# Kernel tuning notes

Hardware: AMD Instinct MI355X
Metric: run time of the kernel (lower is better)

## Reference

```python
import jax, jax.numpy as jnp
import numpy as np

BS, NA, NE_, NL = 128, 3, 3, 3
NALL = NA - 1                 # n_allies
ENT = NA + NE_ + NL           # 9 entities
EM1 = ENT - 1                 # 8
HID = 64                      # hidden_dim
HEAD = 4
HIN = 9                       # hyper input dim
HYP = 64                      # hyper hidden dim
NRBF, RUB = 3, 10.0
EPS = 1e-7


def _lin_init(k, fan_in, fan_out):
    k1, k2 = jax.random.split(k)
    lim = 1.0 / np.sqrt(fan_in)
    w = jax.random.uniform(k1, (fan_in, fan_out), minval=-lim, maxval=lim, dtype=jnp.float32)
    b = jax.random.uniform(k2, (fan_out,), minval=-lim, maxval=lim, dtype=jnp.float32)
    return w, b


def setup_inputs():
    key = jax.random.key(0)
    ks = jax.random.split(key, 12)
    d = {}
    obs_dim = 4 + 2 * (NL + NALL + NE_) + 2 * (NALL + NE_)  # 30
    d["inputs"] = jax.random.normal(ks[0], (BS * NA, obs_dim), dtype=jnp.float32)
    d["hidden_state"] = jnp.zeros((1, HID), dtype=jnp.float32)
    d["actions"] = jax.random.normal(ks[1], (BS * NA, 2), dtype=jnp.float32)
    out_dim = (HIN + 1) * HID * HEAD  # 2560
    d["hA1_w"], d["hA1_b"] = _lin_init(ks[2], HIN, HYP)
    d["hA2_w"], d["hA2_b"] = _lin_init(ks[3], HYP, out_dim)
    d["hE1_w"], d["hE1_b"] = _lin_init(ks[4], HIN, HYP)
    d["hE2_w"], d["hE2_b"] = _lin_init(ks[5], HYP, out_dim)
    d["hL1_w"], d["hL1_b"] = _lin_init(ks[6], HIN, HYP)
    d["hL2_w"], d["hL2_b"] = _lin_init(ks[7], HYP, out_dim)
    d["merger_w"] = jnp.ones((1, HEAD, HID), dtype=jnp.float32)
    d["fc1_w"], d["fc1_b"] = _lin_init(ks[8], HID + 3, HID)
    d["fc2_w"], d["fc2_b"] = _lin_init(ks[9], HID, 1)
    return d


def _pair_out(feat, w1, b1, w2, b2):
    # hypernetwork: Linear(9,64) -> LeakyReLU -> Linear(64, (9+1)*64*4)
    h = jax.nn.leaky_relu(feat @ w1 + b1, negative_slope=0.01)
    out = h @ w2 + b2                               # (bs,NA,EM1,EM1,2560)
    nw = HIN * HID * HEAD
    w = out[..., :nw].reshape(feat.shape[:-1] + (HIN, HID * HEAD))
    b = out[..., nw:]
    y = jnp.einsum('...k,...kd->...d', feat, w) + b  # tiny 1x9 @ 9x256 per pair
    return y.reshape(feat.shape[:-1] + (HEAD, HID))


def _forward(inputs, actions, hA1_w, hA1_b, hA2_w, hA2_b, hE1_w, hE1_b, hE2_w, hE2_b,
             hL1_w, hL1_b, hL2_w, hL2_b, merger_w, fc1_w, fc1_b, fc2_w, fc2_b):
    bs = inputs.shape[0] // NA
    ob = inputs
    own = ob[:, :4].reshape(bs, NA, 4)
    i = 4
    lm_pos = ob[:, i:i + NL * 2].reshape(bs, NA, NL, 2); i += NL * 2
    ally_pos = ob[:, i:i + NALL * 2].reshape(bs, NA, NALL, 2); i += NALL * 2
    enemy_pos = ob[:, i:i + NE_ * 2].reshape(bs, NA, NE_, 2); i += NE_ * 2
    entity_pos = jnp.concatenate([ally_pos, enemy_pos, lm_pos], axis=-2)  # (bs,NA,EM1,2)
    ally_vel = ob[:, i:i + NALL * 2].reshape(bs, NA, NALL, 2); i += NALL * 2
    enemy_vel = ob[:, i:i + NE_ * 2].reshape(bs, NA, NE_, 2)
    lm_vel = jnp.zeros_like(lm_pos) - own[:, :, None, :2]
    entity_vel = jnp.concatenate([ally_vel, enemy_vel, lm_vel], axis=-2)  # (bs,NA,EM1,2)
    # rel_vel[b,a,j,i] = vel[i] - vel[j]
    rel_vel = entity_vel[:, :, None, :, :] - entity_vel[:, :, :, None, :]
    vel_norm = jnp.sqrt((entity_vel ** 2).sum(-1))
    sin_a = entity_vel[..., 1] / (vel_norm + EPS)
    cos_a = entity_vel[..., 0] / (vel_norm + EPS)
    act = actions.reshape(bs, NA, 2)
    act_norm = jnp.sqrt((act ** 2).sum(-1))        # (bs,NA)
    sin_b = act[..., 1] / (act_norm + EPS)
    cos_b = act[..., 0] / (act_norm + EPS)
    dist = jnp.sqrt((entity_pos ** 2).sum(-1))     # (bs,NA,EM1)
    sin_t = entity_pos[..., 1] / (dist + EPS)
    cos_t = entity_pos[..., 0] / (dist + EPS)
    # pair angles: A,C vary over last axis (i), B over second-to-last (j)
    sA, cA = sin_t[:, :, None, :], cos_t[:, :, None, :]
    sB, cB = sin_t[:, :, :, None], cos_t[:, :, :, None]
    sC, cC = sin_a[:, :, None, :], cos_a[:, :, None, :]
    angle_info = jnp.stack([sA * cB - cA * sB, cA * cB + sA * sB,
                            sC * cB - cC * sB, cC * cB + sC * sB], axis=-1)
    angle_info = jnp.broadcast_to(angle_info, (bs, NA, EM1, EM1, 4))
    sD, cD = sin_b[:, :, None], cos_b[:, :, None]
    act_angle = jnp.stack([sD * cos_t - cD * sin_t, cD * cos_t + sD * sin_t], axis=-1)  # (bs,NA,EM1,2)
    # gaussian RBF (schnet-style smearing, num_rbf=3, rbound_upper=10)
    offset = jnp.linspace(0.0, RUB, NRBF)
    coeff = -0.5 / (offset[1] - offset[0]) ** 2
    rbf = jnp.exp(coeff * (dist[..., None] - offset) ** 2)  # (bs,NA,EM1,NRBF)
    feat_dist = jnp.broadcast_to(rbf[:, :, None, :, :], (bs, NA, EM1, EM1, NRBF))
    feat = jnp.concatenate([feat_dist, angle_info, rel_vel], axis=-1)  # (bs,NA,EM1,EM1,9)
    ally_out = _pair_out(feat, hA1_w, hA1_b, hA2_w, hA2_b)
    enemy_out = _pair_out(feat, hE1_w, hE1_b, hE2_w, hE2_b)
    lm_out = _pair_out(feat, hL1_w, hL1_b, hL2_w, hL2_b)
    # type-based selection over the source-entity axis (dim 3), then sum-aggregate
    m = jnp.concatenate([ally_out[:, :, :, :NALL],
                         enemy_out[:, :, :, NALL:NALL + NE_],
                         lm_out[:, :, :, NALL + NE_:]], axis=3)
    m_sum = m.sum(axis=3)                               # (bs,NA,EM1,HEAD,HID)
    mw = jax.nn.softmax(merger_w, axis=1)               # (1,HEAD,HID)
    m_jki = (mw * m_sum).sum(axis=-2)                   # (bs,NA,EM1,HID)
    an = jnp.broadcast_to(act_norm[:, :, None], (bs, NA, EM1))[..., None]
    final = jnp.concatenate([m_jki, an, act_angle], axis=-1)  # (bs,NA,EM1,HID+3)
    x = jax.nn.relu(final)
    x = jax.nn.relu(x @ fc1_w + fc1_b)
    q = (x @ fc2_w + fc2_b).mean(axis=-2).reshape(-1, 1)  # (bs*NA,1)
    return q, x


def reference(inputs, hidden_state, actions, hA1_w, hA1_b, hA2_w, hA2_b,
              hE1_w, hE1_b, hE2_w, hE2_b, hL1_w, hL1_b, hL2_w, hL2_b,
              merger_w, fc1_w, fc1_b, fc2_w, fc2_b):
    q, x = _forward(inputs, actions, hA1_w, hA1_b, hA2_w, hA2_b,
                    hE1_w, hE1_b, hE2_w, hE2_b, hL1_w, hL1_b, hL2_w, hL2_b,
                    merger_w, fc1_w, fc1_b, fc2_w, fc2_b)
    return q, x
```

## Files before the change

### kernel.cpp

```cpp
#include <hip/hip_runtime.h>
#include <math.h>

#define EPS 1e-7f
#define NETS 3
#define HROWP 384
#define HG    (HROWP/4)
#define GPW   (HG/4)
#define JSTRIDE (NETS*HROWP)
#define W2R_F4_TOT (2*NETS*HG*64)
#define ZPART_OFF 589824

__global__ __launch_bounds__(256) void prep_w2r(
    const float* __restrict__ W2A, const float* __restrict__ b2A,
    const float* __restrict__ W2E, const float* __restrict__ b2E,
    const float* __restrict__ W2L, const float* __restrict__ b2L,
    const float* __restrict__ merger, float* __restrict__ W2r)
{
    int idx = blockIdx.x * 256 + threadIdx.x;
    if (idx >= W2R_F4_TOT) return;
    int half = idx / (NETS*HG*64);
    int rem  = idx - half * (NETS*HG*64);
    int net  = rem / (HG*64);
    rem     -= net * (HG*64);
    int g4   = rem >> 6;
    int hid  = rem & 63;

    float m0 = merger[hid], m1 = merger[64+hid], m2 = merger[128+hid], m3 = merger[192+hid];
    float mx = fmaxf(fmaxf(m0, m1), fmaxf(m2, m3));
    float e0 = expf(m0-mx), e1 = expf(m1-mx), e2 = expf(m2-mx), e3 = expf(m3-mx);
    float inv = 1.0f / (e0+e1+e2+e3);
    float w0 = e0*inv, w1 = e1*inv, w2 = e2*inv, w3 = e3*inv;

    const float* W2 = (net==0) ? W2A : ((net==1) ? W2E : W2L);
    const float* b2 = (net==0) ? b2A : ((net==1) ? b2E : b2L);

    float4 v;
    float* vp = &v.x;
    #pragma unroll
    for (int r = 0; r < 4; ++r) {
        int row = g4*4 + r;
        float val = 0.0f;
        if (row < 325) {
            const float* src;
            int kk;
            if (row < 320) { kk = half*5 + (row >> 6); int h = row & 63; src = W2 + h*2560; }
            else           { kk = half*5 + (row - 320);                  src = b2; }
            int col = (kk < 9) ? kk*256 : 2304;
            val = w0*src[col+hid] + w1*src[col+64+hid] + w2*src[col+128+hid] + w3*src[col+192+hid];
        }
        vp[r] = val;
    }
    ((float4*)W2r)[idx] = v;
}

__global__ __launch_bounds__(256, 3) void half_kernel(
    const float* __restrict__ inputs, const float* __restrict__ actions,
    const float* __restrict__ W1A, const float* __restrict__ b1A,
    const float* __restrict__ W1E, const float* __restrict__ b1E,
    const float* __restrict__ W1L, const float* __restrict__ b1L,
    const float* __restrict__ W2r, float* __restrict__ Zpart)
{
    __shared__ float sOb[32];
    __shared__ float sSt[8], sCt[8], sSa[8], sCa[8], sVx[8], sVy[8];
    __shared__ float sRbf[8][3];
    __shared__ __align__(16) float sF2[64][12];
    __shared__ __align__(16) float sU[8 * JSTRIDE];

    const int tid   = threadIdx.x;
    const int agent = blockIdx.x >> 1;
    const int half  = blockIdx.x & 1;
    const int lane  = tid & 63;
    const int w     = tid >> 6;

    float w1r[3][9], b1r[3];
    {
        const float* Ws[3] = {W1A, W1E, W1L};
        const float* bs[3] = {b1A, b1E, b1L};
        #pragma unroll
        for (int net = 0; net < 3; ++net) {
            #pragma unroll
            for (int kk = 0; kk < 9; ++kk) w1r[net][kk] = Ws[net][kk*64 + lane];
            b1r[net] = bs[net][lane];
        }
    }

    if (tid < 30) sOb[tid] = inputs[agent*30 + tid];
    if (tid == 30) sOb[30] = actions[agent*2 + 0];
    if (tid == 31) sOb[31] = actions[agent*2 + 1];
    __syncthreads();

    if (tid < 8) {
        int e = tid;
        float px, py, vx, vy;
        if (e < 2)      {           px = sOb[10+2*e]; py = sOb[11+2*e]; vx = sOb[20+2*e]; vy = sOb[21+2*e]; }
        else if (e < 5) { int t=e-2; px = sOb[14+2*t]; py = sOb[15+2*t]; vx = sOb[24+2*t]; vy = sOb[25+2*t]; }
        else            { int t=e-5; px = sOb[4+2*t];  py = sOb[5+2*t];  vx = -sOb[0];     vy = -sOb[1]; }
        float d  = sqrtf(px*px + py*py);
        sSt[e] = py / (d + EPS);
        sCt[e] = px / (d + EPS);
        float vn = sqrtf(vx*vx + vy*vy);
        sSa[e] = vy / (vn + EPS);
        sCa[e] = vx / (vn + EPS);
        sVx[e] = vx; sVy[e] = vy;
        sRbf[e][0] = expf(-0.02f * d * d);
        float d5  = d - 5.0f;  sRbf[e][1] = expf(-0.02f * d5  * d5);
        float d10 = d - 10.0f; sRbf[e][2] = expf(-0.02f * d10 * d10);
    }
    __syncthreads();

    if (tid < 64) {
        int p = tid, j = p >> 3, k = p & 7;
        sF2[p][0] = sRbf[k][0];
        sF2[p][1] = sRbf[k][1];
        sF2[p][2] = sRbf[k][2];
        sF2[p][3] = sSt[k]*sCt[j] - sCt[k]*sSt[j];
        sF2[p][4] = sCt[k]*sCt[j] + sSt[k]*sSt[j];
        sF2[p][5] = sSa[k]*sCt[j] - sCa[k]*sSt[j];
        sF2[p][6] = sCa[k]*sCt[j] + sSa[k]*sSt[j];
        sF2[p][7] = sVx[k] - sVx[j];
        sF2[p][8] = sVy[k] - sVy[j];
        sF2[p][9] = 1.0f;
        sF2[p][10] = 0.0f;
        sF2[p][11] = 0.0f;
    }
    __syncthreads();

    {
        const int h = lane;
        #pragma unroll
        for (int t = 0; t < 2; ++t) {
            int j = 2*w + t;
            #pragma unroll
            for (int net = 0; net < NETS; ++net) {
                int ks = (net==0) ? 0 : ((net==1) ? 2 : 5);
                int kn = (net==0) ? 2 : 3;
                float v0=0.f,v1=0.f,v2=0.f,v3=0.f,v4=0.f;
                float gs0=0.f,gs1=0.f,gs2=0.f,gs3=0.f,gs4=0.f;
                for (int q = 0; q < kn; ++q) {
                    int p = j*8 + ks + q;
                    float4 fa = *(const float4*)&sF2[p][0];
                    float4 fb = *(const float4*)&sF2[p][4];
                    float4 fc = *(const float4*)&sF2[p][8];
                    float acc = b1r[net];
                    acc = fmaf(fa.x, w1r[net][0], acc);
                    acc = fmaf(fa.y, w1r[net][1], acc);
                    acc = fmaf(fa.z, w1r[net][2], acc);
                    acc = fmaf(fa.w, w1r[net][3], acc);
                    acc = fmaf(fb.x, w1r[net][4], acc);
                    acc = fmaf(fb.y, w1r[net][5], acc);
                    acc = fmaf(fb.z, w1r[net][6], acc);
                    acc = fmaf(fb.w, w1r[net][7], acc);
                    acc = fmaf(fc.x, w1r[net][8], acc);
                    float H = (acc > 0.0f) ? acc : 0.01f*acc;
                    float g0 = half ? fb.y : fa.x;
                    float g1 = half ? fb.z : fa.y;
                    float g2 = half ? fb.w : fa.z;
                    float g3 = half ? fc.x : fa.w;
                    float g4 = half ? fc.y : fb.x;
                    v0 = fmaf(H, g0, v0);  gs0 += g0;
                    v1 = fmaf(H, g1, v1);  gs1 += g1;
                    v2 = fmaf(H, g2, v2);  gs2 += g2;
                    v3 = fmaf(H, g3, v3);  gs3 += g3;
                    v4 = fmaf(H, g4, v4);  gs4 += g4;
                }
                float* dst = sU + (j*NETS + net)*HROWP + h;
                dst[0]   = v0;
                dst[64]  = v1;
                dst[128] = v2;
                dst[192] = v3;
                dst[256] = v4;
                float bv = 0.0f;
                bv = (h==0) ? gs0 : bv;
                bv = (h==1) ? gs1 : bv;
                bv = (h==2) ? gs2 : bv;
                bv = (h==3) ? gs3 : bv;
                bv = (h==4) ? gs4 : bv;
                dst[320 - h + h] = bv;
                sU[(j*NETS + net)*HROWP + 320 + h] = bv;
            }
        }
    }
    __syncthreads();

    float vr[8][4];
    {
        const int q = lane >> 4, hh = lane & 15;
        const int base = w * GPW;
        float acc[8][4];
        #pragma unroll
        for (int j = 0; j < 8; ++j)
            #pragma unroll
            for (int k = 0; k < 4; ++k) acc[j][k] = 0.0f;

        const float4* Wbase = (const float4*)W2r + (size_t)half * (NETS*HG*64);
        float4 wk0, wk1, wk2, wk3;
        {   int g = base + q;
            const float4* wb = Wbase + g*64 + hh;
            wk0 = wb[0]; wk1 = wb[16]; wk2 = wb[32]; wk3 = wb[48]; }

        for (int it = 0; it < 18; ++it) {
            int net = it / 6, u = it - net*6;
            int g = base + u*4 + q;
            float4 nk0, nk1, nk2, nk3;
            if (it < 17) {
                int nit = it + 1;
                int nnet = nit / 6, nu_ = nit - nnet*6;
                int ng = base + nu_*4 + q;
                const float4* wb = Wbase + (nnet*HG + ng)*64 + hh;
                nk0 = wb[0]; nk1 = wb[16]; nk2 = wb[32]; nk3 = wb[48];
            }
            const float* Ub = sU + net*HROWP + g*4;
            #pragma unroll
            for (int j = 0; j < 8; ++j) {
                float4 uu = *(const float4*)(Ub + j*JSTRIDE);
                acc[j][0] = fmaf(uu.x,wk0.x, fmaf(uu.y,wk0.y, fmaf(uu.z,wk0.z, fmaf(uu.w,wk0.w, acc[j][0]))));
                acc[j][1] = fmaf(uu.x,wk1.x, fmaf(uu.y,wk1.y, fmaf(uu.z,wk1.z, fmaf(uu.w,wk1.w, acc[j][1]))));
                acc[j][2] = fmaf(uu.x,wk2.x, fmaf(uu.y,wk2.y, fmaf(uu.z,wk2.z, fmaf(uu.w,wk2.w, acc[j][2]))));
                acc[j][3] = fmaf(uu.x,wk3.x, fmaf(uu.y,wk3.y, fmaf(uu.z,wk3.z, fmaf(uu.w,wk3.w, acc[j][3]))));
            }
            wk0 = nk0; wk1 = nk1; wk2 = nk2; wk3 = nk3;
        }
        #pragma unroll
        for (int j = 0; j < 8; ++j)
            #pragma unroll
            for (int k = 0; k < 4; ++k) {
                float v = acc[j][k];
                v += __shfl_xor(v, 16);
                v += __shfl_xor(v, 32);
                vr[j][k] = v;
            }
    }
    __syncthreads();
    {
        float* sZp = sU;
        const int q = lane >> 4, hh = lane & 15;
        if (q == 0) {
            #pragma unroll
            for (int j = 0; j < 8; ++j)
                #pragma unroll
                for (int k = 0; k < 4; ++k)
                    sZp[(w*8 + j)*64 + k*16 + hh] = vr[j][k];
        }
    }
    __syncthreads();
    {
        const float* sZp = sU;
        float* dst = Zpart + (size_t)agent*1024 + half*512;
        for (int o = tid; o < 512; o += 256)
            dst[o] = sZp[o] + sZp[512+o] + sZp[1024+o] + sZp[1536+o];
    }
}

__global__ __launch_bounds__(256) void epilogue_kernel(
    const float* __restrict__ inputs, const float* __restrict__ actions,
    const float* __restrict__ Zpart,
    const float* __restrict__ fc1w, const float* __restrict__ fc1b,
    const float* __restrict__ fc2w, const float* __restrict__ fc2b,
    float* __restrict__ out_q, float* __restrict__ out_x)
{
    __shared__ float sOb[32];
    __shared__ float sSt[8], sCt[8];
    __shared__ float sAct[3];
    __shared__ float sZ[8][64];
    __shared__ float sRed[4];

    const int tid   = threadIdx.x;
    const int agent = blockIdx.x;

    if (tid < 30) sOb[tid] = inputs[agent*30 + tid];
    if (tid == 30) sOb[30] = actions[agent*2 + 0];
    if (tid == 31) sOb[31] = actions[agent*2 + 1];
    __syncthreads();

    if (tid < 8) {
        int e = tid;
        float px, py;
        if (e < 2)      {           px = sOb[10+2*e]; py = sOb[11+2*e]; }
        else if (e < 5) { int t=e-2; px = sOb[14+2*t]; py = sOb[15+2*t]; }
        else            { int t=e-5; px = sOb[4+2*t];  py = sOb[5+2*t]; }
        float d = sqrtf(px*px + py*py);
        sSt[e] = py / (d + EPS);
        sCt[e] = px / (d + EPS);
    }
    if (tid == 8) {
        float ax = sOb[30], ay = sOb[31];
        float an = sqrtf(ax*ax + ay*ay);
        sAct[0] = an;
        sAct[1] = ay / (an + EPS);
        sAct[2] = ax / (an + EPS);
    }
    const float* Zp = Zpart + (size_t)agent*1024;
    for (int o = tid; o < 512; o += 256) {
        float z = Zp[o] + Zp[512 + o];
        ((float*)sZ)[o] = (z > 0.0f) ? z : 0.0f;
    }
    __syncthreads();

    float an  = sAct[0], sb = sAct[1], cb = sAct[2];
    float anr = (an > 0.0f) ? an : 0.0f;
    float myq = 0.0f;
    #pragma unroll
    for (int i = 0; i < 2; ++i) {
        int o = i*256 + tid;
        int j = o >> 6, c = o & 63;
        float acc = fc1b[c];
        #pragma unroll 8
        for (int d = 0; d < 64; ++d)
            acc = fmaf(sZ[j][d], fc1w[d*64 + c], acc);
        float aa0 = sb*sCt[j] - cb*sSt[j];
        float aa1 = cb*sCt[j] + sb*sSt[j];
        aa0 = (aa0 > 0.0f) ? aa0 : 0.0f;
        aa1 = (aa1 > 0.0f) ? aa1 : 0.0f;
        acc = fmaf(anr, fc1w[64*64 + c], acc);
        acc = fmaf(aa0, fc1w[65*64 + c], acc);
        acc = fmaf(aa1, fc1w[66*64 + c], acc);
        float x1 = (acc > 0.0f) ? acc : 0.0f;
        out_x[(agent*8 + j)*64 + c] = x1;
        myq = fmaf(x1, fc2w[c], myq);
    }
    for (int off = 32; off; off >>= 1) myq += __shfl_down(myq, off);
    int lane = tid & 63, w = tid >> 6;
    if (lane == 0) sRed[w] = myq;
    __syncthreads();
    if (tid == 0) out_q[agent] = (sRed[0] + sRed[1] + sRed[2] + sRed[3]) * 0.125f + fc2b[0];
}

extern "C" void kernel_launch(void* const* d_in, const int* in_sizes, int n_in,
                              void* d_out, int out_size, void* d_ws, size_t ws_size,
                              hipStream_t stream) {
    const float* inputs  = (const float*)d_in[0];
    const float* actions = (const float*)d_in[2];
    const float* hA1_w = (const float*)d_in[3];  const float* hA1_b = (const float*)d_in[4];
    const float* hA2_w = (const float*)d_in[5];  const float* hA2_b = (const float*)d_in[6];
    const float* hE1_w = (const float*)d_in[7];  const float* hE1_b = (const float*)d_in[8];
    const float* hE2_w = (const float*)d_in[9];  const float* hE2_b = (const float*)d_in[10];
    const float* hL1_w = (const float*)d_in[11]; const float* hL1_b = (const float*)d_in[12];
    const float* hL2_w = (const float*)d_in[13]; const float* hL2_b = (const float*)d_in[14];
    const float* merger = (const float*)d_in[15];
    const float* fc1w = (const float*)d_in[16];  const float* fc1b = (const float*)d_in[17];
    const float* fc2w = (const float*)d_in[18];  const float* fc2b = (const float*)d_in[19];

    float* W2r   = (float*)d_ws;
    float* Zpart = (float*)((char*)d_ws + ZPART_OFF);
    float* q     = (float*)d_out;
    float* x     = q + 384;

    prep_w2r<<<(W2R_F4_TOT + 255)/256, 256, 0, stream>>>(
        hA2_w, hA2_b, hE2_w, hE2_b, hL2_w, hL2_b, merger, W2r);
    half_kernel<<<768, 256, 0, stream>>>(
        inputs, actions, hA1_w, hA1_b, hE1_w, hE1_b, hL1_w, hL1_b, W2r, Zpart);
    epilogue_kernel<<<384, 256, 0, stream>>>(
        inputs, actions, Zpart, fc1w, fc1b, fc2w, fc2b, q, x);
}
```

Measured before the change: 120.0 us.

## Compute pair features with wave shuffles and write per-wave partials to global

Pair geometry features are now built entirely in registers with cross-lane shuffles inside each wave, instead of staged through several shared-memory arrays. This removes two block barriers and the shared scratch arrays. The W2 weight prefetch is issued at kernel start so it overlaps the feature computation. The final cross-wave shared reduction and its barriers are also dropped: each wave writes its own partial tile to global memory, and the epilogue kernel sums eight partials instead of two. In exchange, the Zpart scratch buffer grows fourfold and the epilogue does more global reads, so the buffer must be large enough.

After: 121.6 us. About the same (+1.3%).

```diff
diff --git a/kernel.cpp b/kernel.cpp
--- a/kernel.cpp
+++ b/kernel.cpp
@@ -60,10 +60,6 @@
     const float* __restrict__ W1L, const float* __restrict__ b1L,
     const float* __restrict__ W2r, float* __restrict__ Zpart)
 {
-    __shared__ float sOb[32];
-    __shared__ float sSt[8], sCt[8], sSa[8], sCa[8], sVx[8], sVy[8];
-    __shared__ float sRbf[8][3];
-    __shared__ __align__(16) float sF2[64][12];
     __shared__ __align__(16) float sU[8 * JSTRIDE];
 
     const int tid   = threadIdx.x;
@@ -71,6 +67,7 @@
     const int half  = blockIdx.x & 1;
     const int lane  = tid & 63;
     const int w     = tid >> 6;
+    const int q     = lane >> 4, hh = lane & 15;
 
     float w1r[3][9], b1r[3];
     {
@@ -84,170 +81,137 @@
         }
     }
 
-    if (tid < 30) sOb[tid] = inputs[agent*30 + tid];
-    if (tid == 30) sOb[30] = actions[agent*2 + 0];
-    if (tid == 31) sOb[31] = actions[agent*2 + 1];
+    const float4* Wbase = (const float4*)W2r + (size_t)half * (NETS*HG*64);
+    const int base = w * GPW;
+    float4 wk0, wk1, wk2, wk3;
+    {
+        int g = base + q;
+        const float4* wb = Wbase + g*64 + hh;
+        wk0 = wb[0]; wk1 = wb[16]; wk2 = wb[32]; wk3 = wb[48];
+    }
+
+    float ob = 0.0f;
+    if (lane < 30)      ob = inputs[agent*30 + lane];
+    else if (lane < 32) ob = actions[agent*2 + (lane - 30)];
+
+    int e = lane & 7;
+    int ppos, vpos; bool lm = false;
+    if (e < 2)      { ppos = 10+2*e;     vpos = 20+2*e; }
+    else if (e < 5) { ppos = 14+2*(e-2); vpos = 24+2*(e-2); }
+    else            { ppos = 4+2*(e-5);  vpos = 0; lm = true; }
+    float px = __shfl(ob, ppos), py = __shfl(ob, ppos+1);
+    float vx = __shfl(ob, vpos), vy = __shfl(ob, vpos+1);
+    if (lm) { vx = -vx; vy = -vy; }
+    float d  = sqrtf(px*px + py*py);
+    float st = py / (d + EPS), ct = px / (d + EPS);
+    float vn = sqrtf(vx*vx + vy*vy);
+    float sa = vy / (vn + EPS), ca = vx / (vn + EPS);
+    float rb0 = expf(-0.02f * d * d);
+    float d5  = d - 5.0f,  rb1 = expf(-0.02f * d5 * d5);
+    float d10 = d - 10.0f, rb2 = expf(-0.02f * d10 * d10);
+
+    int jj = lane >> 3;
+    float st_j = __shfl(st, jj), ct_j = __shfl(ct, jj);
+    float vx_j = __shfl(vx, jj), vy_j = __shfl(vy, jj);
+    float f0 = rb0, f1 = rb1, f2 = rb2;
+    float f3 = st*ct_j - ct*st_j;
+    float f4 = ct*ct_j + st*st_j;
+    float f5 = sa*ct_j - ca*st_j;
+    float f6 = ca*ct_j + sa*st_j;
+    float f7 = vx - vx_j;
+    float f8 = vy - vy_j;
+
+    #pragma unroll
+    for (int t = 0; t < 2; ++t) {
+        int j = 2*w + t;
+        #pragma unroll
+        for (int net = 0; net < NETS; ++net) {
+            int ks = (net==0) ? 0 : ((net==1) ? 2 : 5);
+            int kn = (net==0) ? 2 : 3;
+            float v0=0.f,v1=0.f,v2=0.f,v3=0.f,v4=0.f;
+            float gs0=0.f,gs1=0.f,gs2=0.f,gs3=0.f,gs4=0.f;
+            for (int qq = 0; qq < kn; ++qq) {
+                int p = j*8 + ks + qq;
+                float s0=__shfl(f0,p), s1=__shfl(f1,p), s2=__shfl(f2,p);
+                float s3=__shfl(f3,p), s4=__shfl(f4,p), s5=__shfl(f5,p);
+                float s6=__shfl(f6,p), s7=__shfl(f7,p), s8=__shfl(f8,p);
+                float acc = b1r[net];
+                acc = fmaf(s0, w1r[net][0], acc);
+                acc = fmaf(s1, w1r[net][1], acc);
+                acc = fmaf(s2, w1r[net][2], acc);
+                acc = fmaf(s3, w1r[net][3], acc);
+                acc = fmaf(s4, w1r[net][4], acc);
+                acc = fmaf(s5, w1r[net][5], acc);
+                acc = fmaf(s6, w1r[net][6], acc);
+                acc = fmaf(s7, w1r[net][7], acc);
+                acc = fmaf(s8, w1r[net][8], acc);
+                float H = (acc > 0.0f) ? acc : 0.01f*acc;
+                float g0 = half ? s5 : s0;
+                float g1 = half ? s6 : s1;
+                float g2 = half ? s7 : s2;
+                float g3 = half ? s8 : s3;
+                float g4 = half ? 1.0f : s4;
+                v0 = fmaf(H, g0, v0);  gs0 += g0;
+                v1 = fmaf(H, g1, v1);  gs1 += g1;
+                v2 = fmaf(H, g2, v2);  gs2 += g2;
+                v3 = fmaf(H, g3, v3);  gs3 += g3;
+                v4 = fmaf(H, g4, v4);  gs4 += g4;
+            }
+            float* dst = sU + (j*NETS + net)*HROWP + lane;
+            dst[0]   = v0;
+            dst[64]  = v1;
+            dst[128] = v2;
+            dst[192] = v3;
+            dst[256] = v4;
+            float bv = 0.0f;
+            bv = (lane==0) ? gs0 : bv;
+            bv = (lane==1) ? gs1 : bv;
+            bv = (lane==2) ? gs2 : bv;
+            bv = (lane==3) ? gs3 : bv;
+            bv = (lane==4) ? gs4 : bv;
+            dst[320] = bv;
+        }
+    }
     __syncthreads();
 
-    if (tid < 8) {
-        int e = tid;
-        float px, py, vx, vy;
-        if (e < 2)      {           px = sOb[10+2*e]; py = sOb[11+2*e]; vx = sOb[20+2*e]; vy = sOb[21+2*e]; }
-        else if (e < 5) { int t=e-2; px = sOb[14+2*t]; py = sOb[15+2*t]; vx = sOb[24+2*t]; vy = sOb[25+2*t]; }
-        else            { int t=e-5; px = sOb[4+2*t];  py = sOb[5+2*t];  vx = -sOb[0];     vy = -sOb[1]; }
-        float d  = sqrtf(px*px + py*py);
-        sSt[e] = py / (d + EPS);
-        sCt[e] = px / (d + EPS);
-        float vn = sqrtf(vx*vx + vy*vy);
-        sSa[e] = vy / (vn + EPS);
-        sCa[e] = vx / (vn + EPS);
-        sVx[e] = vx; sVy[e] = vy;
-        sRbf[e][0] = expf(-0.02f * d * d);
-        float d5  = d - 5.0f;  sRbf[e][1] = expf(-0.02f * d5  * d5);
-        float d10 = d - 10.0f; sRbf[e][2] = expf(-0.02f * d10 * d10);
-    }
-    __syncthreads();
-
-    if (tid < 64) {
-        int p = tid, j = p >> 3, k = p & 7;
-        sF2[p][0] = sRbf[k][0];
-        sF2[p][1] = sRbf[k][1];
-        sF2[p][2] = sRbf[k][2];
-        sF2[p][3] = sSt[k]*sCt[j] - sCt[k]*sSt[j];
-        sF2[p][4] = sCt[k]*sCt[j] + sSt[k]*sSt[j];
-        sF2[p][5] = sSa[k]*sCt[j] - sCa[k]*sSt[j];
-        sF2[p][6] = sCa[k]*sCt[j] + sSa[k]*sSt[j];
-        sF2[p][7] = sVx[k] - sVx[j];
-        sF2[p][8] = sVy[k] - sVy[j];
-        sF2[p][9] = 1.0f;
-        sF2[p][10] = 0.0f;
-        sF2[p][11] = 0.0f;
-    }
-    __syncthreads();
-
-    {
-        const int h = lane;
-        #pragma unroll
-        for (int t = 0; t < 2; ++t) {
-            int j = 2*w + t;
-            #pragma unroll
-            for (int net = 0; net < NETS; ++net) {
-                int ks = (net==0) ? 0 : ((net==1) ? 2 : 5);
-                int kn = (net==0) ? 2 : 3;
-                float v0=0.f,v1=0.f,v2=0.f,v3=0.f,v4=0.f;
-                float gs0=0.f,gs1=0.f,gs2=0.f,gs3=0.f,gs4=0.f;
-                for (int q = 0; q < kn; ++q) {
-                    int p = j*8 + ks + q;
-                    float4 fa = *(const float4*)&sF2[p][0];
-                    float4 fb = *(const float4*)&sF2[p][4];
-                    float4 fc = *(const float4*)&sF2[p][8];
-                    float acc = b1r[net];
-                    acc = fmaf(fa.x, w1r[net][0], acc);
-                    acc = fmaf(fa.y, w1r[net][1], acc);
-                    acc = fmaf(fa.z, w1r[net][2], acc);
-                    acc = fmaf(fa.w, w1r[net][3], acc);
-                    acc = fmaf(fb.x, w1r[net][4], acc);
-                    acc = fmaf(fb.y, w1r[net][5], acc);
-                    acc = fmaf(fb.z, w1r[net][6], acc);
-                    acc = fmaf(fb.w, w1r[net][7], acc);
-                    acc = fmaf(fc.x, w1r[net][8], acc);
-                    float H = (acc > 0.0f) ? acc : 0.01f*acc;
-                    float g0 = half ? fb.y : fa.x;
-                    float g1 = half ? fb.z : fa.y;
-                    float g2 = half ? fb.w : fa.z;
-                    float g3 = half ? fc.x : fa.w;
-                    float g4 = half ? fc.y : fb.x;
-                    v0 = fmaf(H, g0, v0);  gs0 += g0;
-                    v1 = fmaf(H, g1, v1);  gs1 += g1;
-                    v2 = fmaf(H, g2, v2);  gs2 += g2;
-                    v3 = fmaf(H, g3, v3);  gs3 += g3;
-                    v4 = fmaf(H, g4, v4);  gs4 += g4;
-                }
-                float* dst = sU + (j*NETS + net)*HROWP + h;
-                dst[0]   = v0;
-                dst[64]  = v1;
-                dst[128] = v2;
-                dst[192] = v3;
-                dst[256] = v4;
-                float bv = 0.0f;
-                bv = (h==0) ? gs0 : bv;
-                bv = (h==1) ? gs1 : bv;
-                bv = (h==2) ? gs2 : bv;
-                bv = (h==3) ? gs3 : bv;
-                bv = (h==4) ? gs4 : bv;
-                dst[320 - h + h] = bv;
-                sU[(j*NETS + net)*HROWP + 320 + h] = bv;
-            }
-        }
-    }
-    __syncthreads();
-
-    float vr[8][4];
-    {
-        const int q = lane >> 4, hh = lane & 15;
-        const int base = w * GPW;
-        float acc[8][4];
-        #pragma unroll
-        for (int j = 0; j < 8; ++j)
-            #pragma unroll
-            for (int k = 0; k < 4; ++k) acc[j][k] = 0.0f;
-
-        const float4* Wbase = (const float4*)W2r + (size_t)half * (NETS*HG*64);
-        float4 wk0, wk1, wk2, wk3;
-        {   int g = base + q;
-            const float4* wb = Wbase + g*64 + hh;
-            wk0 = wb[0]; wk1 = wb[16]; wk2 = wb[32]; wk3 = wb[48]; }
-
-        for (int it = 0; it < 18; ++it) {
-            int net = it / 6, u = it - net*6;
-            int g = base + u*4 + q;
-            float4 nk0, nk1, nk2, nk3;
-            if (it < 17) {
-                int nit = it + 1;
-                int nnet = nit / 6, nu_ = nit - nnet*6;
-                int ng = base + nu_*4 + q;
-                const float4* wb = Wbase + (nnet*HG + ng)*64 + hh;
-                nk0 = wb[0]; nk1 = wb[16]; nk2 = wb[32]; nk3 = wb[48];
-            }
-            const float* Ub = sU + net*HROWP + g*4;
-            #pragma unroll
-            for (int j = 0; j < 8; ++j) {
-                float4 uu = *(const float4*)(Ub + j*JSTRIDE);
-                acc[j][0] = fmaf(uu.x,wk0.x, fmaf(uu.y,wk0.y, fmaf(uu.z,wk0.z, fmaf(uu.w,wk0.w, acc[j][0]))));
-                acc[j][1] = fmaf(uu.x,wk1.x, fmaf(uu.y,wk1.y, fmaf(uu.z,wk1.z, fmaf(uu.w,wk1.w, acc[j][1]))));
-                acc[j][2] = fmaf(uu.x,wk2.x, fmaf(uu.y,wk2.y, fmaf(uu.z,wk2.z, fmaf(uu.w,wk2.w, acc[j][2]))));
-                acc[j][3] = fmaf(uu.x,wk3.x, fmaf(uu.y,wk3.y, fmaf(uu.z,wk3.z, fmaf(uu.w,wk3.w, acc[j][3]))));
-            }
-            wk0 = nk0; wk1 = nk1; wk2 = nk2; wk3 = nk3;
-        }
-        #pragma unroll
-        for (int j = 0; j < 8; ++j)
-            #pragma unroll
-            for (int k = 0; k < 4; ++k) {
-                float v = acc[j][k];
-                v += __shfl_xor(v, 16);
-                v += __shfl_xor(v, 32);
-                vr[j][k] = v;
-            }
-    }
-    __syncthreads();
-    {
-        float* sZp = sU;
-        const int q = lane >> 4, hh = lane & 15;
-        if (q == 0) {
-            #pragma unroll
-            for (int j = 0; j < 8; ++j)
-                #pragma unroll
-                for (int k = 0; k < 4; ++k)
-                    sZp[(w*8 + j)*64 + k*16 + hh] = vr[j][k];
-        }
-    }
-    __syncthreads();
-    {
-        const float* sZp = sU;
-        float* dst = Zpart + (size_t)agent*1024 + half*512;
-        for (int o = tid; o < 512; o += 256)
-            dst[o] = sZp[o] + sZp[512+o] + sZp[1024+o] + sZp[1536+o];
+    float acc[8][4];
+    #pragma unroll
+    for (int j = 0; j < 8; ++j)
+        #pragma unroll
+        for (int k = 0; k < 4; ++k) acc[j][k] = 0.0f;
+
+    for (int it = 0; it < 18; ++it) {
+        int net = it / 6, u = it - net*6;
+        int g = base + u*4 + q;
+        float4 nk0, nk1, nk2, nk3;
+        if (it < 17) {
+            int nit = it + 1;
+            int nnet = nit / 6, nu_ = nit - nnet*6;
+            int ng = base + nu_*4 + q;
+            const float4* wb = Wbase + (nnet*HG + ng)*64 + hh;
+            nk0 = wb[0]; nk1 = wb[16]; nk2 = wb[32]; nk3 = wb[48];
+        }
+        const float* Ub = sU + net*HROWP + g*4;
+        #pragma unroll
+        for (int j = 0; j < 8; ++j) {
+            float4 uu = *(const float4*)(Ub + j*JSTRIDE);
+            acc[j][0] = fmaf(uu.x,wk0.x, fmaf(uu.y,wk0.y, fmaf(uu.z,wk0.z, fmaf(uu.w,wk0.w, acc[j][0]))));
+            acc[j][1] = fmaf(uu.x,wk1.x, fmaf(uu.y,wk1.y, fmaf(uu.z,wk1.z, fmaf(uu.w,wk1.w, acc[j][1]))));
+            acc[j][2] = fmaf(uu.x,wk2.x, fmaf(uu.y,wk2.y, fmaf(uu.z,wk2.z, fmaf(uu.w,wk2.w, acc[j][2]))));
+            acc[j][3] = fmaf(uu.x,wk3.x, fmaf(uu.y,wk3.y, fmaf(uu.z,wk3.z, fmaf(uu.w,wk3.w, acc[j][3]))));
+        }
+        wk0 = nk0; wk1 = nk1; wk2 = nk2; wk3 = nk3;
+    }
+
+    float* zb = Zpart + (((size_t)agent*2 + half)*4 + w) * 512;
+    #pragma unroll
+    for (int j = 0; j < 8; ++j) {
+        float v0 = acc[j][0]; v0 += __shfl_xor(v0,16); v0 += __shfl_xor(v0,32);
+        float v1 = acc[j][1]; v1 += __shfl_xor(v1,16); v1 += __shfl_xor(v1,32);
+        float v2 = acc[j][2]; v2 += __shfl_xor(v2,16); v2 += __shfl_xor(v2,32);
+        float v3 = acc[j][3]; v3 += __shfl_xor(v3,16); v3 += __shfl_xor(v3,32);
+        float out = (q==0) ? v0 : ((q==1) ? v1 : ((q==2) ? v2 : v3));
+        zb[j*64 + lane] = out;
     }
 }
 
@@ -289,9 +253,11 @@
         sAct[1] = ay / (an + EPS);
         sAct[2] = ax / (an + EPS);
     }
-    const float* Zp = Zpart + (size_t)agent*1024;
+    const float* Zp = Zpart + (size_t)agent*4096;
     for (int o = tid; o < 512; o += 256) {
-        float z = Zp[o] + Zp[512 + o];
+        float z = 0.0f;
+        #pragma unroll
+        for (int c = 0; c < 8; ++c) z += Zp[c*512 + o];
         ((float*)sZ)[o] = (z > 0.0f) ? z : 0.0f;
     }
     __syncthreads();
```
